# Kernel optimization log

Hardware: AMD Instinct MI355X
Metric: run time of the kernel (lower is better)

The kernel has to match this reference:

```python
import jax, jax.numpy as jnp
import numpy as np

NUM_HEADS = 16
ROPE_THETA = 10000.0


def _rotate_half(x):
    d = x.shape[-1] // 2
    return jnp.concatenate((-x[..., d:], x[..., :d]), axis=-1)


def setup_inputs() -> dict:
    key = jax.random.key(0)
    k1, k2, k3, k4 = jax.random.split(key, 4)
    T, HID = 3072, 1024
    hidden_states = jax.random.normal(k1, (T, HID), dtype=jnp.float32)
    w_qkv = jax.random.normal(k2, (HID, 3 * HID), dtype=jnp.float32) * (1.0 / np.sqrt(HID))
    w_o = jax.random.normal(k3, (HID, HID), dtype=jnp.float32) * (1.0 / np.sqrt(HID))
    attention_mask = jnp.zeros((T, T), dtype=jnp.float32)  # additive bias over token pairs
    position_ids = jax.random.randint(k4, (T,), 0, T, dtype=jnp.int32)
    return {
        "hidden_states": hidden_states,
        "w_qkv": w_qkv,
        "w_o": w_o,
        "attention_mask": attention_mask,
        "position_ids": position_ids,
    }


def reference(hidden_states, w_qkv, w_o, attention_mask, position_ids):
    T, hid = hidden_states.shape
    H = NUM_HEADS
    D = hid // H

    # fused QKV projection (bias=False)
    qkv = hidden_states @ w_qkv  # [T, 3*hid]
    q, k, v = jnp.split(qkv, 3, axis=-1)
    q = q.reshape(T, H, D)
    k = k.reshape(T, H, D)
    v = v.reshape(T, H, D)

    # RoPE per packed-token position_ids
    inv_freq = 1.0 / (ROPE_THETA ** (jnp.arange(0, D, 2, dtype=jnp.float32) / D))  # [D/2]
    freqs = position_ids.astype(jnp.float32)[:, None] * inv_freq[None, :]  # [T, D/2]
    emb = jnp.concatenate((freqs, freqs), axis=-1)  # [T, D]
    cos = jnp.cos(emb)[:, None, :]  # [T, 1, D]
    sin = jnp.sin(emb)[:, None, :]
    q = q * cos + _rotate_half(q) * sin
    k = k * cos + _rotate_half(k) * sin

    # dense token-token attention over packed tokens
    scale = 1.0 / np.sqrt(D).astype(np.float32)
    scores = jnp.einsum("thd,shd->hts", q, k) * scale  # [H, T, T]
    scores = scores + attention_mask[None, :, :]
    probs = jax.nn.softmax(scores, axis=-1)
    out = jnp.einsum("hts,shd->thd", probs, v).reshape(T, hid)
    return out @ w_o
```

## Files before the change

kernel.cpp:

```cpp
#include <hip/hip_runtime.h>
#include <hip/hip_bf16.h>
#include <hip/hip_fp16.h>
#include <math.h>

#define T_TOK 3072
#define HID   1024
#define NH    16
#define HD    64
#define KVSPLIT 4
#define KVCHUNK (T_TOK / KVSPLIT)
#define NQB (T_TOK / 128)
#define LOG2E 1.4426950408889634f

typedef __attribute__((ext_vector_type(8))) short bf16x8;
typedef __attribute__((ext_vector_type(8))) unsigned short u16x8;
typedef __attribute__((ext_vector_type(4))) float f32x4;
typedef __attribute__((ext_vector_type(16))) float f32x16;
typedef __attribute__((ext_vector_type(4))) unsigned int u32x4;

#define VMCNT(n) asm volatile("s_waitcnt vmcnt(" #n ")" ::: "memory")
#define SB() __builtin_amdgcn_sched_barrier(0)

static __device__ __forceinline__ unsigned short f2bf(float x) {
  __hip_bfloat16 h = __float2bfloat16(x);
  return __builtin_bit_cast(unsigned short, h);
}
static __device__ __forceinline__ float bf2f(unsigned short u) {
  unsigned int v = (unsigned int)u << 16;
  return __builtin_bit_cast(float, v);
}
static __device__ __forceinline__ unsigned short f2h(float x) {
  __half h = __float2half(x);
  return __builtin_bit_cast(unsigned short, h);
}
static __device__ __forceinline__ float h2f(unsigned short u) {
  __half h = __builtin_bit_cast(__half, u);
  return __half2float(h);
}
static __device__ __forceinline__ unsigned int pack_bf16(float a, float b) {
  unsigned int ua = __builtin_bit_cast(unsigned int, a) + 0x8000u;
  unsigned int ub = __builtin_bit_cast(unsigned int, b) + 0x8000u;
  return (ua >> 16) | (ub & 0xffff0000u);
}

static __device__ __forceinline__ int swz(int row, int cb) {
  return row * 64 + ((cb ^ ((row & 7) << 4)) >> 1);
}

__global__ __launch_bounds__(256) void prep(const float* __restrict__ X,
                                            const float* __restrict__ Wqkv,
                                            const float* __restrict__ Wo,
                                            const int* __restrict__ pos,
                                            const float* __restrict__ mask,
                                            unsigned short* __restrict__ Xb,
                                            unsigned short* __restrict__ WqkvT,
                                            unsigned short* __restrict__ WoT,
                                            float* __restrict__ ctab,
                                            float* __restrict__ stab,
                                            int* __restrict__ flags) {
  __shared__ float tile[32][33];
  __shared__ int sflag;
  const int b = blockIdx.x;
  const int tid = threadIdx.x;
  if (b < 3072) {
    int i = (b * 256 + tid) * 4;
    float4 v = *(const float4*)(X + i);
    ushort4 o;
    o.x = f2bf(v.x); o.y = f2bf(v.y); o.z = f2bf(v.z); o.w = f2bf(v.w);
    *(ushort4*)(Xb + i) = o;
  } else if (b < 6144) {
    int b2 = b - 3072;
    int c0 = (b2 % 96) * 32, r0 = (b2 / 96) * 32;
    int tx = tid & 31, ty = tid >> 5;
    #pragma unroll
    for (int i2 = 0; i2 < 32; i2 += 8)
      tile[ty + i2][tx] = Wqkv[(size_t)(r0 + ty + i2) * 3072 + c0 + tx];
    __syncthreads();
    #pragma unroll
    for (int i2 = 0; i2 < 32; i2 += 8)
      WqkvT[(size_t)(c0 + ty + i2) * 1024 + r0 + tx] = f2bf(tile[tx][ty + i2]);
  } else if (b < 7168) {
    int b2 = b - 6144;
    int c0 = (b2 % 32) * 32, r0 = (b2 / 32) * 32;
    int tx = tid & 31, ty = tid >> 5;
    #pragma unroll
    for (int i2 = 0; i2 < 32; i2 += 8)
      tile[ty + i2][tx] = Wo[(size_t)(r0 + ty + i2) * 1024 + c0 + tx];
    __syncthreads();
    #pragma unroll
    for (int i2 = 0; i2 < 32; i2 += 8)
      WoT[(size_t)(c0 + ty + i2) * 1024 + r0 + tx] = f2bf(tile[tx][ty + i2]);
  } else if (b < 7552) {
    int i = (b - 7168) * 256 + tid;
    int t = i >> 5, j = i & 31;
    float inv = expf(-(float)j * 0.28782313662425572f);
    float f = (float)pos[t] * inv;
    ctab[i] = cosf(f);
    stab[i] = sinf(f);
  } else {
    int c = b - 7552;
    int qx = c % NQB, z = c / NQB;
    const float* base = mask + (size_t)(qx * 128) * T_TOK + z * KVCHUNK;
    int any = 0;
    const int NC4 = KVCHUNK / 4;
    for (int i = tid; i < 128 * NC4; i += 256) {
      int row = i / NC4, cc = i - row * NC4;
      float4 v = *(const float4*)(base + (size_t)row * T_TOK + cc * 4);
      any |= (v.x != 0.f) | (v.y != 0.f) | (v.z != 0.f) | (v.w != 0.f);
    }
    if (tid == 0) sflag = 0;
    __syncthreads();
    if (__any(any) && (tid & 63) == 0) sflag = 1;
    __syncthreads();
    if (tid == 0) flags[z * NQB + qx] = sflag;
  }
}

__global__ __launch_bounds__(256) void gemm_qkv(const unsigned short* __restrict__ A,
                                                const unsigned short* __restrict__ Bt,
                                                const float* __restrict__ ctab,
                                                const float* __restrict__ stab,
                                                unsigned short* __restrict__ Qh,
                                                unsigned short* __restrict__ Kh,
                                                unsigned short* __restrict__ Vt) {
  const int M = T_TOK, N = 3 * HID, K = HID;
  __shared__ unsigned short As[2][128 * 32];
  __shared__ unsigned short Bs[2][128 * 32];
  const int lane = threadIdx.x & 63;
  const int wv = threadIdx.x >> 6;
  const int wm = wv >> 1, wn = wv & 1;
  const int r = lane & 15, hi = lane >> 4;
  const int nwg = gridDim.x;
  const int flat = blockIdx.x;
  const int sid = (flat & 7) * (nwg >> 3) + (flat >> 3);
  const int mblocks = M >> 7;
  const int m0 = (sid % mblocks) * 128, n0 = (sid / mblocks) * 128;

  const int srow = lane >> 2;
  const int scb  = ((lane & 3) * 16) ^ ((srow & 3) << 4);
  const unsigned short* ga = A  + (size_t)(m0 + wv * 16 + srow) * K + (scb >> 1);
  const unsigned short* gb = Bt + (size_t)(n0 + wv * 16 + srow) * K + (scb >> 1);
  char* asd = (char*)&As[0][0] + wv * 1024;
  char* bsd = (char*)&Bs[0][0] + wv * 1024;

  auto stage = [&](int buf, int kt) {
    __builtin_amdgcn_global_load_lds(
        (const __attribute__((address_space(1))) unsigned int*)(ga + kt),
        (__attribute__((address_space(3))) unsigned int*)(asd + buf * 8192), 16, 0, 0);
    __builtin_amdgcn_global_load_lds(
        (const __attribute__((address_space(1))) unsigned int*)(ga + (size_t)64 * K + kt),
        (__attribute__((address_space(3))) unsigned int*)(asd + buf * 8192 + 4096), 16, 0, 0);
    __builtin_amdgcn_global_load_lds(
        (const __attribute__((address_space(1))) unsigned int*)(gb + kt),
        (__attribute__((address_space(3))) unsigned int*)(bsd + buf * 8192), 16, 0, 0);
    __builtin_amdgcn_global_load_lds(
        (const __attribute__((address_space(1))) unsigned int*)(gb + (size_t)64 * K + kt),
        (__attribute__((address_space(3))) unsigned int*)(bsd + buf * 8192 + 4096), 16, 0, 0);
  };

  f32x4 acc[4][4] = {};
  const int NT = K >> 5;
  stage(0, 0);
  #pragma unroll 2
  for (int it = 0; it < NT; ++it) {
    const int buf = it & 1;
    if (it + 1 < NT) {
      stage(buf ^ 1, (it + 1) * 32);
      VMCNT(4);
    } else {
      VMCNT(0);
    }
    SB();
    __builtin_amdgcn_s_barrier();
    SB();
    bf16x8 a[4], b[4];
    const int cbs = (hi * 16) ^ ((r & 3) << 4);
    #pragma unroll
    for (int tm = 0; tm < 4; ++tm)
      a[tm] = *(const bf16x8*)&As[buf][(wm * 64 + tm * 16 + r) * 32 + (cbs >> 1)];
    #pragma unroll
    for (int tn = 0; tn < 4; ++tn)
      b[tn] = *(const bf16x8*)&Bs[buf][(wn * 64 + tn * 16 + r) * 32 + (cbs >> 1)];
    #pragma unroll
    for (int tm = 0; tm < 4; ++tm)
      #pragma unroll
      for (int tn = 0; tn < 4; ++tn)
        acc[tm][tn] = __builtin_amdgcn_mfma_f32_16x16x32_bf16(a[tm], b[tn], acc[tm][tn], 0, 0, 0);
    __builtin_amdgcn_s_barrier();
  }

  const int sec = n0 >> 10;
  const int hh  = ((n0 + wn * 64) >> 6) & 15;
  if (sec < 2) {
    __syncthreads();
    float* ctl = (float*)&As[0][0];
    float* stl = (float*)&Bs[0][0];
    for (int i = threadIdx.x; i < 1024; i += 256) {
      ((float4*)ctl)[i] = *(const float4*)(ctab + (size_t)m0 * 32 + i * 4);
      ((float4*)stl)[i] = *(const float4*)(stab + (size_t)m0 * 32 + i * 4);
    }
    __syncthreads();
    const float qscl = (sec == 0) ? 0.18033688011112042f : 1.0f;
    unsigned short* dst = (sec == 0) ? Qh : Kh;
    #pragma unroll
    for (int tm = 0; tm < 4; ++tm)
      #pragma unroll
      for (int tn2 = 0; tn2 < 2; ++tn2) {
        const int p = tn2 * 16 + r;
        #pragma unroll
        for (int j = 0; j < 4; ++j) {
          int trow = wm * 64 + tm * 16 + hi * 4 + j;
          float c = ctl[trow * 32 + p], s = stl[trow * 32 + p];
          float q1 = acc[tm][tn2][j], q2 = acc[tm][tn2 + 2][j];
          size_t base = ((size_t)hh * T_TOK + (m0 + trow)) * HD + p;
          dst[base]      = f2bf((q1 * c - q2 * s) * qscl);
          dst[base + 32] = f2bf((q2 * c + q1 * s) * qscl);
        }
      }
  } else {
    const int hi2 = ((hi & 1) << 1) | (hi >> 1);
    #pragma unroll
    for (int tn = 0; tn < 4; ++tn) {
      const int d = tn * 16 + r;
      #pragma unroll
      for (int tm = 0; tm < 4; ++tm) {
        int tbase = m0 + wm * 64 + tm * 16 + hi2 * 4;
        ushort4 w;
        w.x = f2bf(acc[tm][tn][0]); w.y = f2bf(acc[tm][tn][1]);
        w.z = f2bf(acc[tm][tn][2]); w.w = f2bf(acc[tm][tn][3]);
        *(ushort4*)(Vt + ((size_t)hh * HD + d) * T_TOK + tbase) = w;
      }
    }
  }
}

__global__ __launch_bounds__(256) void gemm_bt(const unsigned short* __restrict__ A,
                                               const unsigned short* __restrict__ Bt,
                                               float* __restrict__ C, int M, int N, int K) {
  __shared__ unsigned short As[2][128 * 32];
  __shared__ unsigned short Bs[2][128 * 32];
  const int lane = threadIdx.x & 63;
  const int wv = threadIdx.x >> 6;
  const int wm = wv >> 1, wn = wv & 1;
  const int r = lane & 15, hi = lane >> 4;
  const int nwg = gridDim.x;
  const int flat = blockIdx.x;
  const int sid = (flat & 7) * (nwg >> 3) + (flat >> 3);
  const int mblocks = M >> 7;
  const int m0 = (sid % mblocks) * 128, n0 = (sid / mblocks) * 128;

  const int srow = lane >> 2;
  const int scb  = ((lane & 3) * 16) ^ ((srow & 3) << 4);
  const unsigned short* ga = A  + (size_t)(m0 + wv * 16 + srow) * K + (scb >> 1);
  const unsigned short* gb = Bt + (size_t)(n0 + wv * 16 + srow) * K + (scb >> 1);
  char* asd = (char*)&As[0][0] + wv * 1024;
  char* bsd = (char*)&Bs[0][0] + wv * 1024;

  auto stage = [&](int buf, int kt) {
    __builtin_amdgcn_global_load_lds(
        (const __attribute__((address_space(1))) unsigned int*)(ga + kt),
        (__attribute__((address_space(3))) unsigned int*)(asd + buf * 8192), 16, 0, 0);
    __builtin_amdgcn_global_load_lds(
        (const __attribute__((address_space(1))) unsigned int*)(ga + (size_t)64 * K + kt),
        (__attribute__((address_space(3))) unsigned int*)(asd + buf * 8192 + 4096), 16, 0, 0);
    __builtin_amdgcn_global_load_lds(
        (const __attribute__((address_space(1))) unsigned int*)(gb + kt),
        (__attribute__((address_space(3))) unsigned int*)(bsd + buf * 8192), 16, 0, 0);
    __builtin_amdgcn_global_load_lds(
        (const __attribute__((address_space(1))) unsigned int*)(gb + (size_t)64 * K + kt),
        (__attribute__((address_space(3))) unsigned int*)(bsd + buf * 8192 + 4096), 16, 0, 0);
  };

  f32x4 acc[4][4] = {};
  const int NT = K >> 5;
  stage(0, 0);
  #pragma unroll 2
  for (int it = 0; it < NT; ++it) {
    const int buf = it & 1;
    if (it + 1 < NT) {
      stage(buf ^ 1, (it + 1) * 32);
      VMCNT(4);
    } else {
      VMCNT(0);
    }
    SB();
    __builtin_amdgcn_s_barrier();
    SB();
    bf16x8 a[4], b[4];
    const int cbs = (hi * 16) ^ ((r & 3) << 4);
    #pragma unroll
    for (int tm = 0; tm < 4; ++tm)
      a[tm] = *(const bf16x8*)&As[buf][(wm * 64 + tm * 16 + r) * 32 + (cbs >> 1)];
    #pragma unroll
    for (int tn = 0; tn < 4; ++tn)
      b[tn] = *(const bf16x8*)&Bs[buf][(wn * 64 + tn * 16 + r) * 32 + (cbs >> 1)];
    #pragma unroll
    for (int tm = 0; tm < 4; ++tm)
      #pragma unroll
      for (int tn = 0; tn < 4; ++tn)
        acc[tm][tn] = __builtin_amdgcn_mfma_f32_16x16x32_bf16(a[tm], b[tn], acc[tm][tn], 0, 0, 0);
    __builtin_amdgcn_s_barrier();
  }
  #pragma unroll
  for (int tm = 0; tm < 4; ++tm)
    #pragma unroll
    for (int tn = 0; tn < 4; ++tn) {
      int colg = n0 + wn * 64 + tn * 16 + r;
      int rowg = m0 + wm * 64 + tm * 16 + hi * 4;
      float* cp = C + (size_t)rowg * N + colg;
      #pragma unroll
      for (int j = 0; j < 4; ++j) cp[(size_t)j * N] = acc[tm][tn][j];
    }
}

__global__ __launch_bounds__(256) void flash_attn(const unsigned short* __restrict__ Qh,
                                                  const unsigned short* __restrict__ Kh,
                                                  const unsigned short* __restrict__ Vt,
                                                  const float* __restrict__ mask,
                                                  const int* __restrict__ flags,
                                                  unsigned short* __restrict__ Op,
                                                  float* __restrict__ Mp,
                                                  float* __restrict__ Lp) {
  const int NBLK = NH * NQB * KVSPLIT;
  int id = blockIdx.x;
  int sid = (id & 7) * (NBLK / 8) + (id >> 3);
  const int hh = sid / (NQB * KVSPLIT);
  int rem = sid % (NQB * KVSPLIT);
  const int z  = rem / NQB;
  const int qx = rem % NQB;
  const int q0 = qx * 128;
  const int kv0 = z * KVCHUNK;
  const int NT = KVCHUNK / 64;

  __shared__ unsigned short Ks[2][64 * 64];
  __shared__ unsigned short Vs[2][64 * 64];
  const int lane = threadIdx.x & 63, wv = threadIdx.x >> 6;
  const int q31 = lane & 31, h2 = lane >> 5;
  const int qw = q0 + wv * 32 + q31;

  bf16x8 qf[4];
  #pragma unroll
  for (int ks = 0; ks < 4; ++ks)
    qf[ks] = *(const bf16x8*)(Qh + ((size_t)hh * T_TOK + qw) * HD + ks * 16 + h2 * 8);

  f32x16 acc_o[2] = {};
  const int hasmask = flags[z * NQB + qx];
  float m = hasmask ? -INFINITY : 0.f;
  float l = 0.f;

  const int ldrow = lane >> 3;
  const int colS  = ((lane & 7) * 16) ^ (ldrow << 4);
  const unsigned short* kga = Kh + ((size_t)hh * T_TOK + wv * 16 + ldrow) * HD + (colS >> 1);
  const unsigned short* vga = Vt + ((size_t)hh * HD + wv * 16 + ldrow) * T_TOK + (colS >> 1);
  char* ksd = (char*)&Ks[0][0] + wv * 2048;
  char* vsd = (char*)&Vs[0][0] + wv * 2048;
  const float* mrow = mask + (size_t)qw * T_TOK;

  auto stage = [&](int buf, int s0) {
    __builtin_amdgcn_global_load_lds(
        (const __attribute__((address_space(1))) unsigned int*)(kga + (size_t)s0 * HD),
        (__attribute__((address_space(3))) unsigned int*)(ksd + buf * 8192), 16, 0, 0);
    __builtin_amdgcn_global_load_lds(
        (const __attribute__((address_space(1))) unsigned int*)(kga + (size_t)s0 * HD + 8 * HD),
        (__attribute__((address_space(3))) unsigned int*)(ksd + buf * 8192 + 1024), 16, 0, 0);
    __builtin_amdgcn_global_load_lds(
        (const __attribute__((address_space(1))) unsigned int*)(vga + s0),
        (__attribute__((address_space(3))) unsigned int*)(vsd + buf * 8192), 16, 0, 0);
    __builtin_amdgcn_global_load_lds(
        (const __attribute__((address_space(1))) unsigned int*)(vga + s0 + 8 * T_TOK),
        (__attribute__((address_space(3))) unsigned int*)(vsd + buf * 8192 + 1024), 16, 0, 0);
  };

  float4 mk[8];

  auto qkt = [&](int cur, f32x16& as0, f32x16& as1) {
    __builtin_amdgcn_s_setprio(1);
    #pragma unroll
    for (int ks = 0; ks < 4; ++ks) {
      bf16x8 kf0 = *(const bf16x8*)&Ks[cur][swz(q31,      ks * 32 + h2 * 16)];
      bf16x8 kf1 = *(const bf16x8*)&Ks[cur][swz(32 + q31, ks * 32 + h2 * 16)];
      as0 = __builtin_amdgcn_mfma_f32_32x32x16_bf16(kf0, qf[ks], as0, 0, 0, 0);
      as1 = __builtin_amdgcn_mfma_f32_32x32x16_bf16(kf1, qf[ks], as1, 0, 0, 0);
    }
    __builtin_amdgcn_s_setprio(0);
  };

  auto pv = [&](int cur, const unsigned int* pk) {
    __builtin_amdgcn_s_setprio(1);
    #pragma unroll
    for (int kvb = 0; kvb < 2; ++kvb)
      #pragma unroll
      for (int s = 0; s < 2; ++s) {
        u32x4 fr;
        fr[0] = pk[kvb * 8 + 4 * s + 0];
        fr[1] = pk[kvb * 8 + 4 * s + 1];
        fr[2] = pk[kvb * 8 + 4 * s + 2];
        fr[3] = pk[kvb * 8 + 4 * s + 3];
        bf16x8 pfrag = __builtin_bit_cast(bf16x8, fr);
        #pragma unroll
        for (int db = 0; db < 2; ++db) {
          bf16x8 vf = *(const bf16x8*)&Vs[cur][swz(db * 32 + q31, kvb * 64 + s * 32 + h2 * 16)];
          acc_o[db] = __builtin_amdgcn_mfma_f32_32x32x16_bf16(vf, pfrag, acc_o[db], 0, 0, 0);
        }
      }
    __builtin_amdgcn_s_setprio(0);
  };

  auto tile_nomask = [&](int cur) {
    f32x16 as0 = {}, as1 = {};
    qkt(cur, as0, as1);
    float ps = 0.f;
    unsigned int pk[16];
    #pragma unroll
    for (int kvb = 0; kvb < 2; ++kvb) {
      const f32x16& as = kvb ? as1 : as0;
      #pragma unroll
      for (int j = 0; j < 4; ++j) {
        float e0 = __builtin_amdgcn_exp2f(as[j * 4 + 0]);
        float e1 = __builtin_amdgcn_exp2f(as[j * 4 + 1]);
        float e2 = __builtin_amdgcn_exp2f(as[j * 4 + 2]);
        float e3 = __builtin_amdgcn_exp2f(as[j * 4 + 3]);
        ps += (e0 + e1) + (e2 + e3);
        pk[kvb * 8 + j * 2 + 0] = pack_bf16(e0, e1);
        pk[kvb * 8 + j * 2 + 1] = pack_bf16(e2, e3);
      }
    }
    l += ps;
    pv(cur, pk);
  };

  auto tile_mask = [&](int cur) {
    f32x16 as0 = {}, as1 = {};
    qkt(cur, as0, as1);
    float sv[2][16];
    #pragma unroll
    for (int reg = 0; reg < 16; ++reg) {
      float m0v = (&mk[0 + (reg >> 2)].x)[reg & 3];
      float m1v = (&mk[4 + (reg >> 2)].x)[reg & 3];
      sv[0][reg] = fmaf(m0v, LOG2E, as0[reg]);
      sv[1][reg] = fmaf(m1v, LOG2E, as1[reg]);
    }
    float p0 = sv[0][0];
    #pragma unroll
    for (int i = 1; i < 16; ++i) p0 = fmaxf(p0, sv[0][i]);
    #pragma unroll
    for (int i = 0; i < 16; ++i) p0 = fmaxf(p0, sv[1][i]);
    float pmax = fmaxf(p0, __shfl_xor(p0, 32));
    if (__any(pmax > m + 8.f)) {
      float mnew = fmaxf(m, pmax);
      float sc = __builtin_amdgcn_exp2f(m - mnew);
      m = mnew;
      l *= sc;
      #pragma unroll
      for (int db = 0; db < 2; ++db)
        #pragma unroll
        for (int i = 0; i < 16; ++i) acc_o[db][i] *= sc;
    }
    float ps = 0.f;
    unsigned int pk[16];
    #pragma unroll
    for (int kvb = 0; kvb < 2; ++kvb)
      #pragma unroll
      for (int j = 0; j < 4; ++j) {
        float e0 = __builtin_amdgcn_exp2f(sv[kvb][j * 4 + 0] - m);
        float e1 = __builtin_amdgcn_exp2f(sv[kvb][j * 4 + 1] - m);
        float e2 = __builtin_amdgcn_exp2f(sv[kvb][j * 4 + 2] - m);
        float e3 = __builtin_amdgcn_exp2f(sv[kvb][j * 4 + 3] - m);
        ps += (e0 + e1) + (e2 + e3);
        pk[kvb * 8 + j * 2 + 0] = pack_bf16(e0, e1);
        pk[kvb * 8 + j * 2 + 1] = pack_bf16(e2, e3);
      }
    l += ps;
    pv(cur, pk);
  };

  stage(0, kv0);

  if (hasmask) {
    for (int it = 0; it < NT - 1; ++it) {
      const int s0 = kv0 + it * 64;
      #pragma unroll
      for (int kvb = 0; kvb < 2; ++kvb)
        #pragma unroll
        for (int g = 0; g < 4; ++g)
          mk[kvb * 4 + g] = *(const float4*)(mrow + s0 + kvb * 32 + g * 8 + 4 * h2);
      stage((it + 1) & 1, s0 + 64);
      VMCNT(12);
      SB();
      __builtin_amdgcn_s_barrier();
      SB();
      tile_mask(it & 1);
      __builtin_amdgcn_s_barrier();
    }
    const int s0 = kv0 + (NT - 1) * 64;
    #pragma unroll
    for (int kvb = 0; kvb < 2; ++kvb)
      #pragma unroll
      for (int g = 0; g < 4; ++g)
        mk[kvb * 4 + g] = *(const float4*)(mrow + s0 + kvb * 32 + g * 8 + 4 * h2);
    VMCNT(8);
    SB();
    __builtin_amdgcn_s_barrier();
    SB();
    tile_mask((NT - 1) & 1);
  } else {
    for (int it = 0; it < NT - 1; ++it) {
      stage((it + 1) & 1, kv0 + (it + 1) * 64);
      VMCNT(4);
      SB();
      __builtin_amdgcn_s_barrier();
      SB();
      tile_nomask(it & 1);
      __builtin_amdgcn_s_barrier();
    }
    VMCNT(0);
    SB();
    __builtin_amdgcn_s_barrier();
    SB();
    tile_nomask((NT - 1) & 1);
  }

  float lf = l + __shfl_xor(l, 32);
  float lfinv = 1.f / lf;
  unsigned short* oprow = Op + (((size_t)z * T_TOK + qw) * NH + hh) * HD;
  #pragma unroll
  for (int db = 0; db < 2; ++db)
    #pragma unroll
    for (int g = 0; g < 4; ++g) {
      ushort4 o4;
      o4.x = f2h(acc_o[db][g * 4 + 0] * lfinv);
      o4.y = f2h(acc_o[db][g * 4 + 1] * lfinv);
      o4.z = f2h(acc_o[db][g * 4 + 2] * lfinv);
      o4.w = f2h(acc_o[db][g * 4 + 3] * lfinv);
      *(ushort4*)(oprow + db * 32 + g * 8 + 4 * h2) = o4;
    }
  if (h2 == 0) {
    size_t mi = ((size_t)z * T_TOK + qw) * NH + hh;
    Mp[mi] = m;
    Lp[mi] = lf;
  }
}

__global__ __launch_bounds__(256) void combine(const unsigned short* __restrict__ Op,
                                               const float* __restrict__ Mp,
                                               const float* __restrict__ Lp,
                                               unsigned short* __restrict__ Ob) {
  int idx = blockIdx.x * 256 + threadIdx.x;
  int t = idx >> 8;
  int q4 = (idx & 255) * 4;
  int h = q4 >> 6, d = q4 & 63;
  float mz[KVSPLIT], lz[KVSPLIT];
  float ms = -INFINITY;
  #pragma unroll
  for (int zz = 0; zz < KVSPLIT; ++zz) {
    size_t mi = ((size_t)zz * T_TOK + t) * NH + h;
    mz[zz] = Mp[mi];
    lz[zz] = Lp[mi];
    ms = fmaxf(ms, mz[zz]);
  }
  float lsum = 0.f;
  float wl[KVSPLIT];
  #pragma unroll
  for (int zz = 0; zz < KVSPLIT; ++zz) {
    wl[zz] = lz[zz] * __builtin_amdgcn_exp2f(mz[zz] - ms);
    lsum += wl[zz];
  }
  float4 o = {0.f, 0.f, 0.f, 0.f};
  #pragma unroll
  for (int zz = 0; zz < KVSPLIT; ++zz) {
    ushort4 p = *(const ushort4*)(Op + (((size_t)zz * T_TOK + t) * NH + h) * HD + d);
    o.x += h2f(p.x) * wl[zz]; o.y += h2f(p.y) * wl[zz];
    o.z += h2f(p.z) * wl[zz]; o.w += h2f(p.w) * wl[zz];
  }
  float inv = 1.f / lsum;
  ushort4 ob;
  ob.x = f2bf(o.x * inv); ob.y = f2bf(o.y * inv);
  ob.z = f2bf(o.z * inv); ob.w = f2bf(o.w * inv);
  *(ushort4*)(Ob + (size_t)t * HID + q4) = ob;
}

extern "C" void kernel_launch(void* const* d_in, const int* in_sizes, int n_in,
                              void* d_out, int out_size, void* d_ws, size_t ws_size,
                              hipStream_t stream) {
  const float* X    = (const float*)d_in[0];
  const float* Wqkv = (const float*)d_in[1];
  const float* Wo   = (const float*)d_in[2];
  const float* mask = (const float*)d_in[3];
  const int*   pos  = (const int*)d_in[4];
  float* out = (float*)d_out;

  char* ws = (char*)d_ws;
  size_t off = 0;
  auto alloc = [&](size_t bytes) {
    char* p = ws + off;
    off += (bytes + 255) & ~(size_t)255;
    return p;
  };
  unsigned short* Xb    = (unsigned short*)alloc((size_t)T_TOK * HID * 2);
  unsigned short* WqkvT = (unsigned short*)alloc((size_t)3 * HID * HID * 2);
  unsigned short* WoT   = (unsigned short*)alloc((size_t)HID * HID * 2);
  unsigned short* Qh    = (unsigned short*)alloc((size_t)NH * T_TOK * HD * 2);
  unsigned short* Kh    = (unsigned short*)alloc((size_t)NH * T_TOK * HD * 2);
  unsigned short* Vt    = (unsigned short*)alloc((size_t)NH * HD * T_TOK * 2);
  unsigned short* Ob    = (unsigned short*)alloc((size_t)T_TOK * HID * 2);
  float*          ctab  = (float*)alloc((size_t)T_TOK * 32 * 4);
  float*          stab  = (float*)alloc((size_t)T_TOK * 32 * 4);
  float*          Mp    = (float*)alloc((size_t)KVSPLIT * T_TOK * NH * 4);
  float*          Lp    = (float*)alloc((size_t)KVSPLIT * T_TOK * NH * 4);
  int*            flags = (int*)alloc((size_t)KVSPLIT * NQB * 4);
  unsigned short* Op    = (unsigned short*)alloc((size_t)KVSPLIT * T_TOK * HID * 2);

  prep<<<7648, 256, 0, stream>>>(X, Wqkv, Wo, pos, mask, Xb, WqkvT, WoT, ctab, stab, flags);

  gemm_qkv<<<dim3((3 * HID / 128) * (T_TOK / 128)), 256, 0, stream>>>(Xb, WqkvT, ctab, stab, Qh, Kh, Vt);

  flash_attn<<<dim3(NH * NQB * KVSPLIT), 256, 0, stream>>>(Qh, Kh, Vt, mask, flags, Op, Mp, Lp);
  combine<<<T_TOK, 256, 0, stream>>>(Op, Mp, Lp, Ob);

  gemm_bt<<<dim3((HID / 128) * (T_TOK / 128)), 256, 0, stream>>>(Ob, WoT, out, T_TOK, HID, HID);
}
```

Measured before the change: 152.1 us.

## Software-pipeline QK^T of next tile with softmax and PV of current tile

In the unmasked attention path, K and V staging are split so the next tile's K can be fetched earlier. QK^T for tile it+1 is issued before softmax and PV of tile it, using ping-pong accumulators, so MFMA work overlaps the exp and pack work. The aim is to hide softmax latency and load waits behind matrix ops. The cost is more live registers for the second pair of score accumulators, which could lower occupancy, and more complex vmcnt bookkeeping.

```diff
diff --git a/kernel.cpp b/kernel.cpp
--- a/kernel.cpp
+++ b/kernel.cpp
@@ -356,13 +356,15 @@
   char* vsd = (char*)&Vs[0][0] + wv * 2048;
   const float* mrow = mask + (size_t)qw * T_TOK;
 
-  auto stage = [&](int buf, int s0) {
+  auto stageK = [&](int buf, int s0) {
     __builtin_amdgcn_global_load_lds(
         (const __attribute__((address_space(1))) unsigned int*)(kga + (size_t)s0 * HD),
         (__attribute__((address_space(3))) unsigned int*)(ksd + buf * 8192), 16, 0, 0);
     __builtin_amdgcn_global_load_lds(
         (const __attribute__((address_space(1))) unsigned int*)(kga + (size_t)s0 * HD + 8 * HD),
         (__attribute__((address_space(3))) unsigned int*)(ksd + buf * 8192 + 1024), 16, 0, 0);
+  };
+  auto stageV = [&](int buf, int s0) {
     __builtin_amdgcn_global_load_lds(
         (const __attribute__((address_space(1))) unsigned int*)(vga + s0),
         (__attribute__((address_space(3))) unsigned int*)(vsd + buf * 8192), 16, 0, 0);
@@ -370,8 +372,6 @@
         (const __attribute__((address_space(1))) unsigned int*)(vga + s0 + 8 * T_TOK),
         (__attribute__((address_space(3))) unsigned int*)(vsd + buf * 8192 + 1024), 16, 0, 0);
   };
-
-  float4 mk[8];
 
   auto qkt = [&](int cur, f32x16& as0, f32x16& as1) {
     __builtin_amdgcn_s_setprio(1);
@@ -406,11 +406,8 @@
     __builtin_amdgcn_s_setprio(0);
   };
 
-  auto tile_nomask = [&](int cur) {
-    f32x16 as0 = {}, as1 = {};
-    qkt(cur, as0, as1);
+  auto softmax0 = [&](const f32x16& as0, const f32x16& as1, unsigned int* pk) {
     float ps = 0.f;
-    unsigned int pk[16];
     #pragma unroll
     for (int kvb = 0; kvb < 2; ++kvb) {
       const f32x16& as = kvb ? as1 : as0;
@@ -426,57 +423,103 @@
       }
     }
     l += ps;
-    pv(cur, pk);
-  };
-
-  auto tile_mask = [&](int cur) {
-    f32x16 as0 = {}, as1 = {};
-    qkt(cur, as0, as1);
-    float sv[2][16];
-    #pragma unroll
-    for (int reg = 0; reg < 16; ++reg) {
-      float m0v = (&mk[0 + (reg >> 2)].x)[reg & 3];
-      float m1v = (&mk[4 + (reg >> 2)].x)[reg & 3];
-      sv[0][reg] = fmaf(m0v, LOG2E, as0[reg]);
-      sv[1][reg] = fmaf(m1v, LOG2E, as1[reg]);
-    }
-    float p0 = sv[0][0];
-    #pragma unroll
-    for (int i = 1; i < 16; ++i) p0 = fmaxf(p0, sv[0][i]);
-    #pragma unroll
-    for (int i = 0; i < 16; ++i) p0 = fmaxf(p0, sv[1][i]);
-    float pmax = fmaxf(p0, __shfl_xor(p0, 32));
-    if (__any(pmax > m + 8.f)) {
-      float mnew = fmaxf(m, pmax);
-      float sc = __builtin_amdgcn_exp2f(m - mnew);
-      m = mnew;
-      l *= sc;
-      #pragma unroll
-      for (int db = 0; db < 2; ++db)
+  };
+
+  if (!hasmask) {
+    f32x16 aA0 = {}, aA1 = {}, aB0 = {}, aB1 = {};
+    stageK(0, kv0); stageV(0, kv0);
+    stageK(1, kv0 + 64);
+    VMCNT(4);
+    SB(); __builtin_amdgcn_s_barrier(); SB();
+    qkt(0, aA0, aA1);
+    __builtin_amdgcn_s_barrier();
+
+    unsigned int pk[16];
+    for (int it = 0; it < NT; it += 2) {
+      {
+        if (it + 1 < NT) stageV((it + 1) & 1, kv0 + (it + 1) * 64);
+        if (it + 2 < NT) stageK(it & 1,       kv0 + (it + 2) * 64);
+        if (it + 2 < NT)      { VMCNT(4); }
+        else if (it + 1 < NT) { VMCNT(2); }
+        else                  { VMCNT(0); }
+        SB(); __builtin_amdgcn_s_barrier(); SB();
+        if (it + 1 < NT) {
+          aB0 = (f32x16){}; aB1 = (f32x16){};
+          qkt((it + 1) & 1, aB0, aB1);
+        }
+        softmax0(aA0, aA1, pk);
+        pv(it & 1, pk);
+        __builtin_amdgcn_s_barrier();
+      }
+      if (it + 1 < NT) {
+        const int jt = it + 1;
+        if (jt + 1 < NT) stageV((jt + 1) & 1, kv0 + (jt + 1) * 64);
+        if (jt + 2 < NT) stageK(jt & 1,       kv0 + (jt + 2) * 64);
+        if (jt + 2 < NT)      { VMCNT(4); }
+        else if (jt + 1 < NT) { VMCNT(2); }
+        else                  { VMCNT(0); }
+        SB(); __builtin_amdgcn_s_barrier(); SB();
+        if (jt + 1 < NT) {
+          aA0 = (f32x16){}; aA1 = (f32x16){};
+          qkt((jt + 1) & 1, aA0, aA1);
+        }
+        softmax0(aB0, aB1, pk);
+        pv(jt & 1, pk);
+        __builtin_amdgcn_s_barrier();
+      }
+    }
+  } else {
+    auto stage = [&](int buf, int s0) {
+      stageK(buf, s0);
+      stageV(buf, s0);
+    };
+    float4 mk[8];
+    auto tile_mask = [&](int cur) {
+      f32x16 as0 = {}, as1 = {};
+      qkt(cur, as0, as1);
+      float sv[2][16];
+      #pragma unroll
+      for (int reg = 0; reg < 16; ++reg) {
+        float m0v = (&mk[0 + (reg >> 2)].x)[reg & 3];
+        float m1v = (&mk[4 + (reg >> 2)].x)[reg & 3];
+        sv[0][reg] = fmaf(m0v, LOG2E, as0[reg]);
+        sv[1][reg] = fmaf(m1v, LOG2E, as1[reg]);
+      }
+      float p0 = sv[0][0];
+      #pragma unroll
+      for (int i = 1; i < 16; ++i) p0 = fmaxf(p0, sv[0][i]);
+      #pragma unroll
+      for (int i = 0; i < 16; ++i) p0 = fmaxf(p0, sv[1][i]);
+      float pmax = fmaxf(p0, __shfl_xor(p0, 32));
+      if (__any(pmax > m + 8.f)) {
+        float mnew = fmaxf(m, pmax);
+        float sc = __builtin_amdgcn_exp2f(m - mnew);
+        m = mnew;
+        l *= sc;
         #pragma unroll
-        for (int i = 0; i < 16; ++i) acc_o[db][i] *= sc;
-    }
-    float ps = 0.f;
-    unsigned int pk[16];
-    #pragma unroll
-    for (int kvb = 0; kvb < 2; ++kvb)
-      #pragma unroll
-      for (int j = 0; j < 4; ++j) {
-        float e0 = __builtin_amdgcn_exp2f(sv[kvb][j * 4 + 0] - m);
-        float e1 = __builtin_amdgcn_exp2f(sv[kvb][j * 4 + 1] - m);
-        float e2 = __builtin_amdgcn_exp2f(sv[kvb][j * 4 + 2] - m);
-        float e3 = __builtin_amdgcn_exp2f(sv[kvb][j * 4 + 3] - m);
-        ps += (e0 + e1) + (e2 + e3);
-        pk[kvb * 8 + j * 2 + 0] = pack_bf16(e0, e1);
-        pk[kvb * 8 + j * 2 + 1] = pack_bf16(e2, e3);
-      }
-    l += ps;
-    pv(cur, pk);
-  };
-
-  stage(0, kv0);
-
-  if (hasmask) {
+        for (int db = 0; db < 2; ++db)
+          #pragma unroll
+          for (int i = 0; i < 16; ++i) acc_o[db][i] *= sc;
+      }
+      float ps = 0.f;
+      unsigned int pk[16];
+      #pragma unroll
+      for (int kvb = 0; kvb < 2; ++kvb)
+        #pragma unroll
+        for (int j = 0; j < 4; ++j) {
+          float e0 = __builtin_amdgcn_exp2f(sv[kvb][j * 4 + 0] - m);
+          float e1 = __builtin_amdgcn_exp2f(sv[kvb][j * 4 + 1] - m);
+          float e2 = __builtin_amdgcn_exp2f(sv[kvb][j * 4 + 2] - m);
+          float e3 = __builtin_amdgcn_exp2f(sv[kvb][j * 4 + 3] - m);
+          ps += (e0 + e1) + (e2 + e3);
+          pk[kvb * 8 + j * 2 + 0] = pack_bf16(e0, e1);
+          pk[kvb * 8 + j * 2 + 1] = pack_bf16(e2, e3);
+        }
+      l += ps;
+      pv(cur, pk);
+    };
+
+    stage(0, kv0);
     for (int it = 0; it < NT - 1; ++it) {
       const int s0 = kv0 + it * 64;
       #pragma unroll
@@ -503,21 +546,6 @@
     __builtin_amdgcn_s_barrier();
     SB();
     tile_mask((NT - 1) & 1);
-  } else {
-    for (int it = 0; it < NT - 1; ++it) {
-      stage((it + 1) & 1, kv0 + (it + 1) * 64);
-      VMCNT(4);
-      SB();
-      __builtin_amdgcn_s_barrier();
-      SB();
-      tile_nomask(it & 1);
-      __builtin_amdgcn_s_barrier();
-    }
-    VMCNT(0);
-    SB();
-    __builtin_amdgcn_s_barrier();
-    SB();
-    tile_nomask((NT - 1) & 1);
   }
 
   float lf = l + __shfl_xor(l, 32);
```

Result: faster. 148.5 us (-2.4%).
